# Optimization experiments

Measured on AMD Instinct MI355X. Metric: run time of the kernel, lower is better.

## Reference

```python
import jax, jax.numpy as jnp
import numpy as np

HEADS = 12
EMBED = 768
HEAD_DIM = EMBED // HEADS
SCALING = HEAD_DIM ** (-0.5)


def setup_inputs() -> dict:
    key = jax.random.key(0)
    k1, k2, k3, k4, k5 = jax.random.split(key, 5)
    B, N = 8, 1024
    x = jax.random.normal(k1, (B, N, EMBED), dtype=jnp.float32)
    W_qkv = jax.random.normal(k2, (3 * EMBED, EMBED), dtype=jnp.float32) * 0.02
    b_qkv = jax.random.normal(k3, (3 * EMBED,), dtype=jnp.float32) * 0.02
    W_proj = jax.random.normal(k4, (EMBED, EMBED), dtype=jnp.float32) * 0.02
    b_proj = jax.random.normal(k5, (EMBED,), dtype=jnp.float32) * 0.02
    return {"x": x, "W_qkv": W_qkv, "b_qkv": b_qkv, "W_proj": W_proj, "b_proj": b_proj}


def reference(x, W_qkv, b_qkv, W_proj, b_proj):
    B, N, D = x.shape
    # fused QKV projection: [B, N, 3D]
    qkv = x @ W_qkv.T + b_qkv
    # split last dim as (u=3, h, e) per einops 'b n (u h e) -> u b h n e'
    qkv = qkv.reshape(B, N, 3, HEADS, HEAD_DIM).transpose(2, 0, 3, 1, 4)
    q, k, v = qkv[0], qkv[1], qkv[2]
    # raw dot-product scores (NO pre-softmax scaling, per original)
    sim = jnp.einsum('bhqi,bhki->bhqk', q, k)
    # unusual POST-softmax scaling
    sim = jax.nn.softmax(sim, axis=-1) * SCALING
    att = jnp.einsum('bhnk,bhke->bhne', sim, v)
    att = att.transpose(0, 2, 1, 3).reshape(B, N, D)  # b h n e -> b n (h e)
    return att @ W_proj.T + b_proj
```

## Files before the change

### kernel.cpp

```cpp
#include <hip/hip_runtime.h>

typedef unsigned short u16;
typedef __attribute__((ext_vector_type(8))) short bf16x8;
typedef __attribute__((ext_vector_type(4))) float f32x4;

#define HEADS 12
#define HDIM  64
#define EMBED 768
#define TD    2304
#define SEQ   1024
#define MTOK  8192
#define GK    768
#define GNT   12
#define LOG2E 1.4426950408889634f

#if __has_builtin(__builtin_amdgcn_exp2f)
#define EXP2(x) __builtin_amdgcn_exp2f(x)
#else
#define EXP2(x) exp2f(x)
#endif

__device__ __forceinline__ u16 f2bf(float f) {
  union { float f; unsigned u; } x; x.f = f;
  unsigned r = x.u + 0x7fffu + ((x.u >> 16) & 1u);
  return (u16)(r >> 16);
}

__device__ __forceinline__ unsigned cvt_pk_bf16(float lo, float hi) {
  unsigned r;
  asm("v_cvt_pk_bf16_f32 %0, %1, %2" : "=v"(r) : "v"(lo), "v"(hi));
  return r;
}

__global__ void cast3_kernel(const float* __restrict__ x, const float* __restrict__ wq,
                             const float* __restrict__ wp, u16* __restrict__ xb,
                             u16* __restrict__ wqb, u16* __restrict__ wpb) {
  const int N1 = MTOK * EMBED / 4, N2 = TD * EMBED / 4, N3 = EMBED * EMBED / 4;
  int i = blockIdx.x * blockDim.x + threadIdx.x;
  int st = gridDim.x * blockDim.x;
  for (; i < N1 + N2 + N3; i += st) {
    const float* s; u16* d; int j;
    if (i < N1)           { s = x;  d = xb;  j = i; }
    else if (i < N1 + N2) { s = wq; d = wqb; j = i - N1; }
    else                  { s = wp; d = wpb; j = i - N1 - N2; }
    float4 v = reinterpret_cast<const float4*>(s)[j];
    ushort4 o;
    o.x = f2bf(v.x); o.y = f2bf(v.y); o.z = f2bf(v.z); o.w = f2bf(v.w);
    reinterpret_cast<ushort4*>(d)[j] = o;
  }
}

__device__ __forceinline__ void gload_lds16(const u16* g, u16* l) {
  __builtin_amdgcn_global_load_lds(
      (const __attribute__((address_space(1))) unsigned*)g,
      (__attribute__((address_space(3))) unsigned*)l, 16, 0, 0);
}

__device__ __forceinline__ void memfence_bar() {
  asm volatile("" ::: "memory");
  __builtin_amdgcn_s_barrier();
  asm volatile("" ::: "memory");
}

__global__ __launch_bounds__(256, 2) void gemm_qkv(const u16* __restrict__ A,
                                                   const u16* __restrict__ B,
                                                   const float* __restrict__ bias,
                                                   u16* __restrict__ Cq,
                                                   u16* __restrict__ vt) {
  __shared__ u16 As[3][128 * 64];
  __shared__ u16 Bs[2][96 * 64];
  const int tid  = threadIdx.x;
  const int wave = tid >> 6, lane = tid & 63;
  const int wr = wave >> 1, wc = wave & 1;
  const int lr = lane & 15, g = lane >> 4;

  const int swz = (blockIdx.x & 7) * 64 + (blockIdx.x >> 3);
  const int ny = swz & 7, mx = swz >> 3;

  const u16* Ag = A + (size_t)(mx * 128) * GK;

  const int srow   = lane >> 3;
  const int schunk = (lane & 7) ^ srow;

  auto stageA = [&](int u) {
    u16* dst = As[u % 3];
    const int k0 = (u % GNT) * 64;
#pragma unroll
    for (int c = 0; c < 4; ++c) {
      int slot = wave * 4 + c;
      int row  = slot * 8 + srow;
      gload_lds16(Ag + (size_t)row * GK + k0 + schunk * 8, &dst[slot * 512]);
    }
  };
  auto stageB = [&](int u) {
    u16* dst = Bs[u & 1];
    const int k0 = (u % GNT) * 64;
    const u16* Bg = B + (size_t)((ny + (u / GNT) * 8) * 96) * GK;
#pragma unroll
    for (int c = 0; c < 3; ++c) {
      int slot = wave * 3 + c;
      int row  = slot * 8 + srow;
      gload_lds16(Bg + (size_t)row * GK + k0 + schunk * 8, &dst[slot * 512]);
    }
  };

  f32x4 acc[4][3];
#pragma unroll
  for (int m = 0; m < 4; ++m)
#pragma unroll
    for (int n = 0; n < 3; ++n) acc[m][n] = 0.f;

  const int TOT = 3 * GNT;
  stageA(0);
  stageB(0);
  stageA(1);
  asm volatile("s_waitcnt vmcnt(4)" ::: "memory");
  memfence_bar();

  for (int u = 0; u < TOT; ++u) {
    if (u + 1 < TOT) stageB(u + 1);
    if (u + 2 < TOT) stageA(u + 2);

    const u16* Ab = As[u % 3];
    const u16* Bb = Bs[u & 1];
    bf16x8 af[4][2], bfr[3][2];
#pragma unroll
    for (int m = 0; m < 4; ++m)
#pragma unroll
      for (int kk = 0; kk < 2; ++kk) {
        int r = wr * 64 + m * 16 + lr;
        af[m][kk] = *reinterpret_cast<const bf16x8*>(
            &Ab[r * 64 + (((kk * 4 + g) ^ (r & 7)) << 3)]);
      }
#pragma unroll
    for (int n = 0; n < 3; ++n)
#pragma unroll
      for (int kk = 0; kk < 2; ++kk) {
        int r = wc * 48 + n * 16 + lr;
        bfr[n][kk] = *reinterpret_cast<const bf16x8*>(
            &Bb[r * 64 + (((kk * 4 + g) ^ (r & 7)) << 3)]);
      }

    __builtin_amdgcn_s_setprio(1);
#pragma unroll
    for (int m = 0; m < 4; ++m)
#pragma unroll
      for (int n = 0; n < 3; ++n) {
        acc[m][n] = __builtin_amdgcn_mfma_f32_16x16x32_bf16(bfr[n][0], af[m][0], acc[m][n], 0, 0, 0);
        acc[m][n] = __builtin_amdgcn_mfma_f32_16x16x32_bf16(bfr[n][1], af[m][1], acc[m][n], 0, 0, 0);
      }
    __builtin_amdgcn_s_setprio(0);

    if (u + 3 <= TOT) {
      asm volatile("s_waitcnt vmcnt(4)" ::: "memory");
      memfence_bar();
    } else if (u + 2 == TOT) {
      asm volatile("s_waitcnt vmcnt(0)" ::: "memory");
      memfence_bar();
    }

    if ((u % GNT) == GNT - 1) {
      const int seg = u / GNT;
      const int row0 = mx * 128 + wr * 64 + lr;
      const int colb = (ny + seg * 8) * 96 + wc * 48 + g * 4;
      if (seg < 2) {
        const float sc = (seg == 0) ? LOG2E : 1.f;
#pragma unroll
        for (int m = 0; m < 4; ++m)
#pragma unroll
          for (int n = 0; n < 3; ++n) {
            int row = row0 + m * 16;
            int col = colb + n * 16;
            float4 bv = *reinterpret_cast<const float4*>(&bias[col]);
            ushort4 pw;
            pw.x = f2bf((acc[m][n][0] + bv.x) * sc);
            pw.y = f2bf((acc[m][n][1] + bv.y) * sc);
            pw.z = f2bf((acc[m][n][2] + bv.z) * sc);
            pw.w = f2bf((acc[m][n][3] + bv.w) * sc);
            *reinterpret_cast<ushort4*>(&Cq[(size_t)row * TD + col]) = pw;
            acc[m][n] = 0.f;
          }
      } else {
#pragma unroll
        for (int m = 0; m < 4; ++m) {
          int row = row0 + m * 16;
          int b   = row >> 10;
          int tk  = row & 1023;
#pragma unroll
          for (int n = 0; n < 3; ++n) {
            int col = colb + n * 16;
            float4 bv = *reinterpret_cast<const float4*>(&bias[col]);
#pragma unroll
            for (int j = 0; j < 4; ++j) {
              int vcol = col + j - 2 * EMBED;
              int h = vcol >> 6, e = vcol & 63;
              float v = acc[m][n][j] + (j == 0 ? bv.x : j == 1 ? bv.y : j == 2 ? bv.z : bv.w);
              vt[((size_t)(b * HEADS + h) * HDIM + e) * SEQ + tk] = f2bf(v);
            }
            acc[m][n] = 0.f;
          }
        }
      }
    }
  }
}

template <bool OUT_BF16>
__global__ __launch_bounds__(256, 2) void gemm_min2(const u16* __restrict__ A,
                                                    const u16* __restrict__ B,
                                                    const float* __restrict__ bias,
                                                    void* __restrict__ Cv,
                                                    int NBN, int Ndim) {
  __shared__ u16 As[3][128 * 64];
  __shared__ u16 Bs[2][96 * 64];
  const int tid  = threadIdx.x;
  const int wave = tid >> 6, lane = tid & 63;
  const int wr = wave >> 1, wc = wave & 1;
  const int lr = lane & 15, g = lane >> 4;

  const int nwg = gridDim.x;
  const int swz = (blockIdx.x & 7) * (nwg >> 3) + (blockIdx.x >> 3);
  const int ny = swz % NBN, mx = swz / NBN;

  const u16* Ag = A + (size_t)(mx * 128) * GK;
  const u16* Bg = B + (size_t)(ny * 96) * GK;

  const int srow   = lane >> 3;
  const int schunk = (lane & 7) ^ srow;

  auto stageA = [&](int kt) {
    u16* dst = As[kt % 3];
#pragma unroll
    for (int c = 0; c < 4; ++c) {
      int slot = wave * 4 + c;
      int row  = slot * 8 + srow;
      gload_lds16(Ag + (size_t)row * GK + kt * 64 + schunk * 8, &dst[slot * 512]);
    }
  };
  auto stageB = [&](int kt) {
    u16* dst = Bs[kt & 1];
#pragma unroll
    for (int c = 0; c < 3; ++c) {
      int slot = wave * 3 + c;
      int row  = slot * 8 + srow;
      gload_lds16(Bg + (size_t)row * GK + kt * 64 + schunk * 8, &dst[slot * 512]);
    }
  };

  f32x4 acc[4][3];
#pragma unroll
  for (int m = 0; m < 4; ++m)
#pragma unroll
    for (int n = 0; n < 3; ++n) acc[m][n] = 0.f;

  stageA(0);
  stageB(0);
  stageA(1);
  asm volatile("s_waitcnt vmcnt(4)" ::: "memory");
  memfence_bar();

  for (int t = 0; t < GNT; ++t) {
    if (t + 1 < GNT) stageB(t + 1);
    if (t + 2 < GNT) stageA(t + 2);

    const u16* Ab = As[t % 3];
    const u16* Bb = Bs[t & 1];
    bf16x8 af[4][2], bfr[3][2];
#pragma unroll
    for (int m = 0; m < 4; ++m)
#pragma unroll
      for (int kk = 0; kk < 2; ++kk) {
        int r = wr * 64 + m * 16 + lr;
        af[m][kk] = *reinterpret_cast<const bf16x8*>(
            &Ab[r * 64 + (((kk * 4 + g) ^ (r & 7)) << 3)]);
      }
#pragma unroll
    for (int n = 0; n < 3; ++n)
#pragma unroll
      for (int kk = 0; kk < 2; ++kk) {
        int r = wc * 48 + n * 16 + lr;
        bfr[n][kk] = *reinterpret_cast<const bf16x8*>(
            &Bb[r * 64 + (((kk * 4 + g) ^ (r & 7)) << 3)]);
      }

    __builtin_amdgcn_s_setprio(1);
#pragma unroll
    for (int m = 0; m < 4; ++m)
#pragma unroll
      for (int n = 0; n < 3; ++n) {
        acc[m][n] = __builtin_amdgcn_mfma_f32_16x16x32_bf16(bfr[n][0], af[m][0], acc[m][n], 0, 0, 0);
        acc[m][n] = __builtin_amdgcn_mfma_f32_16x16x32_bf16(bfr[n][1], af[m][1], acc[m][n], 0, 0, 0);
      }
    __builtin_amdgcn_s_setprio(0);

    if (t + 3 <= GNT) {
      asm volatile("s_waitcnt vmcnt(4)" ::: "memory");
      memfence_bar();
    } else if (t + 2 == GNT) {
      asm volatile("s_waitcnt vmcnt(0)" ::: "memory");
      memfence_bar();
    }
  }

  const int row0 = mx * 128 + wr * 64 + lr;
  const int col0 = ny * 96 + wc * 48 + g * 4;
#pragma unroll
  for (int m = 0; m < 4; ++m)
#pragma unroll
    for (int n = 0; n < 3; ++n) {
      int row = row0 + m * 16;
      int col = col0 + n * 16;
      float4 bv = *reinterpret_cast<const float4*>(&bias[col]);
      float v0 = acc[m][n][0] + bv.x, v1 = acc[m][n][1] + bv.y;
      float v2 = acc[m][n][2] + bv.z, v3 = acc[m][n][3] + bv.w;
      if (OUT_BF16) {
        ushort4 pw;
        pw.x = f2bf(v0); pw.y = f2bf(v1); pw.z = f2bf(v2); pw.w = f2bf(v3);
        *reinterpret_cast<ushort4*>(&((u16*)Cv)[(size_t)row * Ndim + col]) = pw;
      } else {
        *reinterpret_cast<float4*>(&((float*)Cv)[(size_t)row * Ndim + col]) =
            make_float4(v0, v1, v2, v3);
      }
    }
}

__global__ __launch_bounds__(256, 3) void attn_kernel(const u16* __restrict__ qkv,
                                                      const u16* __restrict__ vt,
                                                      u16* __restrict__ ctx) {
  const int bh = blockIdx.x;
  const int b = bh / HEADS, h = bh % HEADS;
  const int qt = blockIdx.y;
  const int tid = threadIdx.x, wave = tid >> 6, lane = tid & 63;
  const int lr = lane & 15, g = lane >> 4;

  __shared__ u16 Ks[2][64 * 64];
  __shared__ u16 Vs[2][64 * 64];
  __shared__ u16 Ps[128 * 64];

  const size_t tok0 = (size_t)b * SEQ;
  const int q0 = qt * 128;
  const int mbase = wave * 32;

  bf16x8 qf[2][2];
#pragma unroll
  for (int mi = 0; mi < 2; ++mi)
#pragma unroll
    for (int dk = 0; dk < 2; ++dk)
      qf[mi][dk] = *reinterpret_cast<const bf16x8*>(
          qkv + (tok0 + q0 + mbase + mi * 16 + lr) * TD + h * HDIM + dk * 32 + g * 8);

  const int srow = lane >> 3;
  const int schunk = (lane & 7) ^ srow;
  const u16* vbase = vt + (size_t)bh * (HDIM * SEQ);

  auto stage = [&](int kb, int buf) {
#pragma unroll
    for (int c2 = 0; c2 < 2; ++c2) {
      int call = wave * 2 + c2;
      int row  = call * 8 + srow;
      gload_lds16(qkv + (tok0 + kb * 64 + row) * TD + EMBED + h * HDIM + schunk * 8,
                  &Ks[buf][call * 512]);
      gload_lds16(vbase + (size_t)row * SEQ + kb * 64 + schunk * 8,
                  &Vs[buf][call * 512]);
    }
  };

  f32x4 oacc[2][4];
#pragma unroll
  for (int mi = 0; mi < 2; ++mi)
#pragma unroll
    for (int e = 0; e < 4; ++e) oacc[mi][e] = 0.f;
  float psum[2] = {0.f, 0.f};

  stage(0, 0);
  asm volatile("s_waitcnt vmcnt(0)" ::: "memory");
  memfence_bar();

  int cur = 0;
  for (int kb = 0; kb < 16; ++kb) {
    if (kb < 15) stage(kb + 1, cur ^ 1);

    bf16x8 ka[4][2], vb2[4][2];
#pragma unroll
    for (int n = 0; n < 4; ++n)
#pragma unroll
      for (int dk = 0; dk < 2; ++dk) {
        int r = n * 16 + lr;
        int c = dk * 4 + g;
        ka[n][dk]  = *reinterpret_cast<const bf16x8*>(&Ks[cur][r * 64 + ((c ^ (r & 7)) << 3)]);
        vb2[n][dk] = *reinterpret_cast<const bf16x8*>(&Vs[cur][r * 64 + ((c ^ (r & 7)) << 3)]);
      }

#pragma unroll
    for (int mi = 0; mi < 2; ++mi) {
      int m = mbase + mi * 16 + lr;
      int pswz = (lr & 7) << 1;
#pragma unroll
      for (int n = 0; n < 4; ++n) {
        f32x4 s = 0.f;
        __builtin_amdgcn_s_setprio(1);
        s = __builtin_amdgcn_mfma_f32_16x16x32_bf16(ka[n][0], qf[mi][0], s, 0, 0, 0);
        s = __builtin_amdgcn_mfma_f32_16x16x32_bf16(ka[n][1], qf[mi][1], s, 0, 0, 0);
        __builtin_amdgcn_s_setprio(0);
        float e0 = EXP2(s[0]), e1 = EXP2(s[1]);
        float e2 = EXP2(s[2]), e3 = EXP2(s[3]);
        psum[mi] += (e0 + e1) + (e2 + e3);
        uint2 pw;
        pw.x = cvt_pk_bf16(e0, e1);
        pw.y = cvt_pk_bf16(e2, e3);
        int gran = n * 4 + g;
        *reinterpret_cast<uint2*>(&Ps[m * 64 + ((gran ^ pswz) << 2)]) = pw;
      }
    }

#pragma unroll
    for (int mi = 0; mi < 2; ++mi) {
      bf16x8 pa[2];
#pragma unroll
      for (int kk = 0; kk < 2; ++kk) {
        int r = mbase + mi * 16 + lr;
        int c = kk * 4 + g;
        pa[kk] = *reinterpret_cast<const bf16x8*>(&Ps[r * 64 + ((c ^ (r & 7)) << 3)]);
      }
      __builtin_amdgcn_s_setprio(1);
#pragma unroll
      for (int e = 0; e < 4; ++e) {
        oacc[mi][e] = __builtin_amdgcn_mfma_f32_16x16x32_bf16(pa[0], vb2[e][0], oacc[mi][e], 0, 0, 0);
        oacc[mi][e] = __builtin_amdgcn_mfma_f32_16x16x32_bf16(pa[1], vb2[e][1], oacc[mi][e], 0, 0, 0);
      }
      __builtin_amdgcn_s_setprio(0);
    }

    if (kb < 15) {
      asm volatile("s_waitcnt vmcnt(0)" ::: "memory");
      memfence_bar();
    }
    cur ^= 1;
  }

  float scl[2][4];
#pragma unroll
  for (int mi = 0; mi < 2; ++mi) {
    float v = psum[mi];
    v += __shfl_xor(v, 16);
    v += __shfl_xor(v, 32);
    v = 0.125f / v;
#pragma unroll
    for (int j = 0; j < 4; ++j) scl[mi][j] = __shfl(v, 4 * g + j);
  }
#pragma unroll
  for (int mi = 0; mi < 2; ++mi)
#pragma unroll
    for (int e = 0; e < 4; ++e)
#pragma unroll
      for (int j = 0; j < 4; ++j) {
        float v = oacc[mi][e][j] * scl[mi][j];
        ctx[(tok0 + q0 + mbase + mi * 16 + 4 * g + j) * EMBED + h * HDIM + e * 16 + lr] = f2bf(v);
      }
}

extern "C" void kernel_launch(void* const* d_in, const int* in_sizes, int n_in,
                              void* d_out, int out_size, void* d_ws, size_t ws_size,
                              hipStream_t stream) {
  (void)in_sizes; (void)n_in; (void)out_size;
  const float* x     = (const float*)d_in[0];
  const float* Wqkv  = (const float*)d_in[1];
  const float* bqkv  = (const float*)d_in[2];
  const float* Wproj = (const float*)d_in[3];
  const float* bproj = (const float*)d_in[4];
  float* out = (float*)d_out;

  char* ws = (char*)d_ws;
  size_t off = 0;
  auto alloc = [&](size_t bytes) {
    char* p = ws + off;
    off += (bytes + 255) & ~(size_t)255;
    return p;
  };
  u16* xb     = (u16*)alloc((size_t)MTOK * EMBED * 2);
  u16* wqkvb  = (u16*)alloc((size_t)TD * EMBED * 2);
  u16* wprojb = (u16*)alloc((size_t)EMBED * EMBED * 2);
  u16* qkvb   = (u16*)alloc((size_t)MTOK * TD * 2);
  u16* ctxb   = (u16*)alloc((size_t)MTOK * EMBED * 2);
  u16* vtb    = (u16*)alloc((size_t)MTOK * EMBED * 2);
  if (off > ws_size) return;

  cast3_kernel<<<dim3(2048), dim3(256), 0, stream>>>(x, Wqkv, Wproj, xb, wqkvb, wprojb);

  gemm_qkv<<<dim3(512), dim3(256), 0, stream>>>(xb, wqkvb, bqkv, qkvb, vtb);
  attn_kernel<<<dim3(96, 8), dim3(256), 0, stream>>>(qkvb, vtb, ctxb);
  gemm_min2<false><<<dim3(512), dim3(256), 0, stream>>>(ctxb, wprojb, bproj, out, 8, EMBED);
}
```

Before: 113.3 us.

## Triple-buffer K tiles with staggered prefetch and shrink P scratch buffer

Result: no change. 112.8 us (-0.4%).

```diff
diff --git a/kernel.cpp b/kernel.cpp
--- a/kernel.cpp
+++ b/kernel.cpp
@@ -333,9 +333,9 @@
   const int tid = threadIdx.x, wave = tid >> 6, lane = tid & 63;
   const int lr = lane & 15, g = lane >> 4;
 
-  __shared__ u16 Ks[2][64 * 64];
+  __shared__ u16 Ks[3][64 * 64];
   __shared__ u16 Vs[2][64 * 64];
-  __shared__ u16 Ps[128 * 64];
+  __shared__ u16 Ps[64 * 64];
 
   const size_t tok0 = (size_t)b * SEQ;
   const int q0 = qt * 128;
@@ -353,15 +353,24 @@
   const int schunk = (lane & 7) ^ srow;
   const u16* vbase = vt + (size_t)bh * (HDIM * SEQ);
 
-  auto stage = [&](int kb, int buf) {
+  auto stageK = [&](int kb) {
+    u16* dst = Ks[kb % 3];
 #pragma unroll
     for (int c2 = 0; c2 < 2; ++c2) {
       int call = wave * 2 + c2;
       int row  = call * 8 + srow;
       gload_lds16(qkv + (tok0 + kb * 64 + row) * TD + EMBED + h * HDIM + schunk * 8,
-                  &Ks[buf][call * 512]);
+                  &dst[call * 512]);
+    }
+  };
+  auto stageV = [&](int kb) {
+    u16* dst = Vs[kb & 1];
+#pragma unroll
+    for (int c2 = 0; c2 < 2; ++c2) {
+      int call = wave * 2 + c2;
+      int row  = call * 8 + srow;
       gload_lds16(vbase + (size_t)row * SEQ + kb * 64 + schunk * 8,
-                  &Vs[buf][call * 512]);
+                  &dst[call * 512]);
     }
   };
 
@@ -372,14 +381,18 @@
     for (int e = 0; e < 4; ++e) oacc[mi][e] = 0.f;
   float psum[2] = {0.f, 0.f};
 
-  stage(0, 0);
-  asm volatile("s_waitcnt vmcnt(0)" ::: "memory");
+  stageK(0);
+  stageV(0);
+  stageK(1);
+  asm volatile("s_waitcnt vmcnt(2)" ::: "memory");
   memfence_bar();
 
-  int cur = 0;
   for (int kb = 0; kb < 16; ++kb) {
-    if (kb < 15) stage(kb + 1, cur ^ 1);
-
+    if (kb + 1 < 16) stageV(kb + 1);
+    if (kb + 2 < 16) stageK(kb + 2);
+
+    const u16* Kb = Ks[kb % 3];
+    const u16* Vb = Vs[kb & 1];
     bf16x8 ka[4][2], vb2[4][2];
 #pragma unroll
     for (int n = 0; n < 4; ++n)
@@ -387,14 +400,14 @@
       for (int dk = 0; dk < 2; ++dk) {
         int r = n * 16 + lr;
         int c = dk * 4 + g;
-        ka[n][dk]  = *reinterpret_cast<const bf16x8*>(&Ks[cur][r * 64 + ((c ^ (r & 7)) << 3)]);
-        vb2[n][dk] = *reinterpret_cast<const bf16x8*>(&Vs[cur][r * 64 + ((c ^ (r & 7)) << 3)]);
-      }
-
+        ka[n][dk]  = *reinterpret_cast<const bf16x8*>(&Kb[r * 64 + ((c ^ (r & 7)) << 3)]);
+        vb2[n][dk] = *reinterpret_cast<const bf16x8*>(&Vb[r * 64 + ((c ^ (r & 7)) << 3)]);
+      }
+
+    const int m = wave * 16 + lr;
+    const int pswz = (lr & 7) << 1;
 #pragma unroll
     for (int mi = 0; mi < 2; ++mi) {
-      int m = mbase + mi * 16 + lr;
-      int pswz = (lr & 7) << 1;
 #pragma unroll
       for (int n = 0; n < 4; ++n) {
         f32x4 s = 0.f;
@@ -411,16 +424,11 @@
         int gran = n * 4 + g;
         *reinterpret_cast<uint2*>(&Ps[m * 64 + ((gran ^ pswz) << 2)]) = pw;
       }
-    }
-
-#pragma unroll
-    for (int mi = 0; mi < 2; ++mi) {
       bf16x8 pa[2];
 #pragma unroll
       for (int kk = 0; kk < 2; ++kk) {
-        int r = mbase + mi * 16 + lr;
         int c = kk * 4 + g;
-        pa[kk] = *reinterpret_cast<const bf16x8*>(&Ps[r * 64 + ((c ^ (r & 7)) << 3)]);
+        pa[kk] = *reinterpret_cast<const bf16x8*>(&Ps[m * 64 + ((c ^ (m & 7)) << 3)]);
       }
       __builtin_amdgcn_s_setprio(1);
 #pragma unroll
@@ -431,11 +439,13 @@
       __builtin_amdgcn_s_setprio(0);
     }
 
-    if (kb < 15) {
+    if (kb <= 13) {
+      asm volatile("s_waitcnt vmcnt(2)" ::: "memory");
+      memfence_bar();
+    } else if (kb == 14) {
       asm volatile("s_waitcnt vmcnt(0)" ::: "memory");
       memfence_bar();
     }
-    cur ^= 1;
   }
 
   float scl[2][4];
```
